# Optimization experiments

Measured on AMD Instinct MI355X. Metric: run time of the kernel, lower is better.

## Reference

```python
import jax, jax.numpy as jnp
import numpy as np
from jax import lax

N_SIN = 3

def _bn(x, g, b, m, v, eps):
    sh = [1] * x.ndim; sh[1] = -1
    r = lambda t: t.reshape(sh)
    return (x - r(m)) / jnp.sqrt(r(v) + eps) * r(g) + r(b)

def _conv2d(x, w, b, padding):
    y = lax.conv_general_dilated(x, w, (1, 1), padding,
                                 dimension_numbers=('NCHW', 'OIHW', 'NCHW'))
    return y + b[None, :, None, None]

def _causal_conv1d(x, w, b):
    k = w.shape[-1]
    y = lax.conv_general_dilated(x, w, (1,), [(k - 1, 0)],
                                 dimension_numbers=('NCH', 'OIH', 'NCH'))
    return y + b[None, :, None]

def _se(x, w1, w2):
    y = x.mean(axis=2)                                   # [B,C] global avg pool
    y = jax.nn.sigmoid(jax.nn.relu(y @ w1.T) @ w2.T)
    return x * y[:, :, None]

def _kan(x, W1, W2, B1, B2):
    # x: [B,din]; per-edge tiny MLP: sin/cos embed -> linear -> silu -> linear
    omega = (2.0 ** jnp.arange(N_SIN)).astype(x.dtype)   # [n_sin]
    ox = x[..., None] * omega                            # [B,din,n_sin]
    feat = jnp.concatenate([x[..., None], jnp.sin(ox), jnp.cos(ox)], axis=-1)  # [B,din,7]
    h = jnp.einsum('bif,ijhf->bijh', feat, W1) + B1[None]  # [B,din,dout,h]
    h = jax.nn.silu(h)
    out = jnp.einsum('bijh,ijh->bij', h, W2[:, :, 0, :]) + B2[None, :, :, 0]
    return out.sum(axis=1)                               # [B,dout]

def _lstm(x, w_ih, w_hh, b_ih, b_hh):
    B, T, E = x.shape
    H = w_hh.shape[1]
    def step(carry, xt):
        h, c = carry
        g = xt @ w_ih.T + h @ w_hh.T + (b_ih + b_hh)
        i, f, gg, o = jnp.split(g, 4, axis=-1)           # torch gate order i,f,g,o
        c = jax.nn.sigmoid(f) * c + jax.nn.sigmoid(i) * jnp.tanh(gg)
        h = jax.nn.sigmoid(o) * jnp.tanh(c)
        return (h, c), h
    init = (jnp.zeros((B, H), x.dtype), jnp.zeros((B, H), x.dtype))
    _, hs = lax.scan(step, init, jnp.swapaxes(x, 0, 1))
    return jnp.swapaxes(hs, 0, 1)                        # [B,T,H]

def _cluster(hidden):
    B, T, H = hidden.shape
    last = hidden[:, -1, :]
    hn = hidden / jnp.maximum(jnp.linalg.norm(hidden, axis=-1, keepdims=True), 1e-8)
    sim = jnp.einsum('bth,bsh->bts', hn, hn)
    sim = jnp.exp(-5.5 * (1.0 - sim))
    sim = sim * (1.0 - jnp.eye(T, dtype=sim.dtype))      # zero diagonal
    # 2-D prefix sums replace the O(T) python loop over block means
    S = jnp.cumsum(jnp.cumsum(sim, axis=1), axis=2)
    Sii = jnp.diagonal(S, axis1=1, axis2=2)[:, :T - 1]   # sum of [:i,:i]
    R = S[:, -1, :T - 1]                                 # sum of [:, :i]
    C = S[:, :T - 1, -1]                                 # sum of [:i, :]
    tot = S[:, -1, -1][:, None]
    i_f = jnp.arange(1, T, dtype=sim.dtype)
    dist = (Sii / i_f**2
            + (tot - R - C + Sii) / (T - i_f)**2
            - (C - Sii) / (i_f * (T - i_f))
            - (R - Sii) / (i_f * (T - i_f)))             # [B,T-1]
    cuts = jnp.argmax(dist, axis=1) + 1                  # [B]
    mask = (jnp.arange(T)[None, :] < cuts[:, None]).astype(hidden.dtype)
    corr = (hidden * mask[:, :, None]).sum(axis=1) / cuts[:, None].astype(hidden.dtype)
    return last, corr

def reference(x, we1, be1, bn_e1_g, bn_e1_b, bn_e1_m, bn_e1_v, we2, be2, bn_e2_g, bn_e2_b, bn_e2_m, bn_e2_v, w_ih, w_hh, b_ih, b_hh, mu_W1, mu_W2, mu_B1, mu_B2, std_W1, std_W2, std_B1, std_B2, muc_W1, muc_W2, muc_B1, muc_B2, stdc_W1, stdc_W2, stdc_B1, stdc_B2, fc_W1, fc_W2, fc_B1, fc_B2, wc1, bc1, bn1_g, bn1_b, bn1_m, bn1_v, se1_w1, se1_w2, wc2, bc2, bn2_g, bn2_b, bn2_m, bn2_v, se2_w1, se2_w2, wc3, bc3, bn3_g, bn3_b, bn3_m, bn3_v, eps1, eps2):
    gelu = lambda t: jax.nn.gelu(t, approximate=False)
    x = jnp.transpose(x, (0, 2, 1))                      # shuffle: [B,T,F]->[B,F,T]
    h2d = _conv2d(x[:, None], we1, be1, 'SAME')          # [B,4E,F,T]
    h2d = gelu(_bn(h2d, bn_e1_g, bn_e1_b, bn_e1_m, bn_e1_v, 1e-5))
    h2d = _conv2d(h2d, we2, be2, 'VALID')                # [B,E,1,T]
    h2d = gelu(_bn(h2d, bn_e2_g, bn_e2_b, bn_e2_m, bn_e2_v, 1e-5))
    x_src = jnp.transpose(h2d[:, :, 0, :], (0, 2, 1))    # [B,T,E]
    hseq = _lstm(x_src, w_ih, w_hh, b_ih, b_hh)          # [B,T,H]
    out, corr = _cluster(hseq)
    mu = _kan(corr, mu_W1, mu_W2, mu_B1, mu_B2)
    std = jax.nn.softplus(_kan(corr, std_W1, std_W2, std_B1, std_B2) - 5.0)
    z = mu + std * eps1
    x_z = jnp.concatenate([out, z], axis=1)              # [B,2H]
    mu_c = _kan(x_z, muc_W1, muc_W2, muc_B1, muc_B2)
    std_c = jax.nn.softplus(_kan(x_z, stdc_W1, stdc_W2, stdc_B1, stdc_B2) - 5.0)
    x1 = mu_c + std_c * eps2                             # dropout = identity (eval)
    x2 = jnp.transpose(x, (0, 2, 1))                     # [B,T,F]: channels = seq_len
    x2 = gelu(_bn(_causal_conv1d(x2, wc1, bc1), bn1_g, bn1_b, bn1_m, bn1_v, 1e-3))
    x2 = _se(x2, se1_w1, se1_w2)
    x2 = gelu(_bn(_causal_conv1d(x2, wc2, bc2), bn2_g, bn2_b, bn2_m, bn2_v, 1e-3))
    x2 = _se(x2, se2_w1, se2_w2)
    x2 = gelu(_bn(_causal_conv1d(x2, wc3, bc3), bn3_g, bn3_b, bn3_m, bn3_v, 1e-3))
    x2 = x2.mean(axis=2)                                 # [B,conv3_nf]
    x_all = jnp.concatenate([x1, x2], axis=1)            # [B, H+conv3_nf]
    return _kan(x_all, fc_W1, fc_W2, fc_B1, fc_B2)       # [B,num_classes]

def setup_inputs():
    key = jax.random.key(0)
    ks = iter(jax.random.split(key, 128))
    f32 = jnp.float32
    def n(shape, s=0.05):
        return s * jax.random.normal(next(ks), shape, f32)
    def bn_params(c):
        g = 1.0 + 0.05 * jax.random.normal(next(ks), (c,), f32)
        b = 0.05 * jax.random.normal(next(ks), (c,), f32)
        m = 0.05 * jax.random.normal(next(ks), (c,), f32)
        v = jax.random.uniform(next(ks), (c,), f32, 0.5, 1.5)
        return g, b, m, v
    def kan_params(din, dout, h=32, feat=1 + 2 * N_SIN):
        s = (2.0 / (feat + h)) ** 0.5
        return (n((din, dout, h, feat), s), n((din, dout, 1, h), s),
                jnp.zeros((din, dout, h), f32), jnp.zeros((din, dout, 1), f32))
    B, T, F_, E, H = 32, 256, 32, 64, 128
    inp = {}
    inp['x'] = jax.random.normal(next(ks), (B, T, F_), f32)
    inp['we1'] = n((4 * E, 1, 1, 8)); inp['be1'] = n((4 * E,))
    inp['bn_e1_g'], inp['bn_e1_b'], inp['bn_e1_m'], inp['bn_e1_v'] = bn_params(4 * E)
    inp['we2'] = n((E, 4 * E, F_, 1)); inp['be2'] = n((E,))
    inp['bn_e2_g'], inp['bn_e2_b'], inp['bn_e2_m'], inp['bn_e2_v'] = bn_params(E)
    inp['w_ih'] = n((4 * H, E)); inp['w_hh'] = n((4 * H, H))
    inp['b_ih'] = n((4 * H,)); inp['b_hh'] = n((4 * H,))
    for nm, (di, do) in [('mu', (H, H)), ('std', (H, H)), ('muc', (2 * H, H)), ('stdc', (2 * H, H)), ('fc', (2 * H, 10))]:
        w1, w2, b1, b2 = kan_params(di, do)
        inp[nm + '_W1'], inp[nm + '_W2'], inp[nm + '_B1'], inp[nm + '_B2'] = w1, w2, b1, b2
    inp['wc1'] = n((128, T, 8)); inp['bc1'] = n((128,))
    inp['bn1_g'], inp['bn1_b'], inp['bn1_m'], inp['bn1_v'] = bn_params(128)
    inp['se1_w1'] = n((8, 128)); inp['se1_w2'] = n((128, 8))
    inp['wc2'] = n((256, 128, 5)); inp['bc2'] = n((256,))
    inp['bn2_g'], inp['bn2_b'], inp['bn2_m'], inp['bn2_v'] = bn_params(256)
    inp['se2_w1'] = n((16, 256)); inp['se2_w2'] = n((256, 16))
    inp['wc3'] = n((128, 256, 3)); inp['bc3'] = n((128,))
    inp['bn3_g'], inp['bn3_b'], inp['bn3_m'], inp['bn3_v'] = bn_params(128)
    inp['eps1'] = jax.random.normal(next(ks), (B, H), f32)
    inp['eps2'] = jax.random.normal(next(ks), (B, H), f32)
    return inp
```

## Files before the change

kernel.cpp:

```cpp
#include <hip/hip_runtime.h>
#include <hip/hip_bf16.h>
#include <math.h>

typedef __hip_bfloat16 bf16;

#define DEV static __device__ __forceinline__

DEV float geluf(float x){ return 0.5f*x*(1.0f + erff(x*0.70710678118654752f)); }
DEV float sigmf(float x){ return 1.0f/(1.0f + __expf(-x)); }
DEV float softplusf(float x){ return (x > 15.f) ? x : log1pf(__expf(x)); }
DEV float tanhfast(float x){ float e = __expf(2.f*x); return fmaf(-2.f, 1.f/(e+1.f), 1.f); }

typedef __attribute__((ext_vector_type(8))) short v8s;
typedef __attribute__((ext_vector_type(4))) float v4f;
typedef _Float16 f16;
typedef f16 h2 __attribute__((ext_vector_type(2)));
typedef f16 f16x8 __attribute__((ext_vector_type(8)));
typedef unsigned u32x4 __attribute__((ext_vector_type(4)));

DEV float dot2f(h2 a, h2 b, float c){
#if __has_builtin(__builtin_amdgcn_fdot2)
  return __builtin_amdgcn_fdot2(a, b, c, false);
#else
  return fmaf((float)a.y, (float)b.y, fmaf((float)a.x, (float)b.x, c));
// ... 150 lines not shown
  for(int i=tid;i<2048;i+=256) w1s[i] = w1f[i];
  b1s[tid] = b1f[tid];
  for(int i=tid;i<39*32;i+=256){
    int r=i>>5, f=i&31; int t=t0-3+r;
    xs[i] = (t>=0 && t<256) ? x[(b*256+t)*32+f] : 0.f;
  }
  __syncthreads();

  int f = tid & 31, tq = tid >> 5;
  int lane = tid & 63, w = tid >> 6;
  int wm = w & 1, wn = w >> 1;
  int m0 = wm*16, n0 = wn*32;
  int l15 = lane & 15, quad = lane >> 4;

  const v8s* Wv = (const v8s*)Wr;

  auto stage = [&](int cc, int buf){
    v8s bw[4];
    #pragma unroll
    for(int i=0;i<4;i++) bw[i] = Wv[cc*1024 + i*256 + tid];
    unsigned short aval[16];
    #pragma unroll
    for(int ol=0;ol<4;ol++){
      int o = cc*4 + ol;
      float wv[8];
      #pragma unroll
      for(int j=0;j<8;j++) wv[j] = w1s[o*8+j];
      float bb = b1s[o];
      #pragma unroll
      for(int i=0;i<4;i++){
        int tl = tq*4 + i;
        float c = bb;
        #pragma unroll
        for(int j=0;j<8;j++) c = fmaf(wv[j], xs[(tl+j)*32+f], c);
        aval[ol*4+i] = ((__hip_bfloat16_raw)__float2bfloat16(geluf(c))).x;
      }
    }
    #pragma unroll
    for(int ol=0;ol<4;ol++){
      #pragma unroll
      for(int i=0;i<4;i++)
        At[buf][(tq*4+i)*136 + ol*32 + f] = aval[ol*4+i];
    }
    #pragma unroll
    for(int i=0;i<4;i++){
      int j = i*256 + tid;
      int ol = j>>8, e = (j&255)>>2, f8 = j&3;
      *(v8s*)&Bt[buf][ol*2560 + e*40 + f8*8] = bw[i];
    }
  };

  stage(0, 0);
  __syncthreads();

  v4f acc0 = {0.f,0.f,0.f,0.f}, acc1 = {0.f,0.f,0.f,0.f};

  for(int c=0;c<64;c++){
    int p = c & 1, q = p ^ 1;
    if(c < 63) stage(c+1, q);
    #pragma unroll
    for(int ol=0;ol<4;ol++){
      v8s av = *(const v8s*)&At[p][(m0+l15)*136 + ol*32 + quad*8];
      v8s b0 = *(const v8s*)&Bt[p][ol*2560 + (n0+l15)*40 + quad*8];
      v8s b1 = *(const v8s*)&Bt[p][ol*2560 + (n0+16+l15)*40 + quad*8];
      acc0 = __builtin_amdgcn_mfma_f32_16x16x32_bf16(av, b0, acc0, 0, 0, 0);
      acc1 = __builtin_amdgcn_mfma_f32_16x16x32_bf16(av, b1, acc1, 0, 0, 0);
    }
    __syncthreads();
  }

  #pragma unroll
  for(int r=0;r<4;r++){
    int t = t0 + m0 + quad*4 + r;
    int e0 = n0 + l15;
    float v0 = geluf(s2e[e0]*acc0[r] + b2e[e0]);
    x_src[((size_t)(b*256+t))*64 + e0] = v0;
    int e1 = e0 + 16;
    float v1 = geluf(s2e[e1]*acc1[r] + b2e[e1]);
    x_src[((size_t)(b*256+t))*64 + e1] = v1;
  }
}

__global__ __launch_bounds__(256) void gates_kernel(
    const float* x_src, const float* wihT, const float* biasg, float* gx)
{
  __shared__ float xsh[32*64];
  int blk = blockIdx.x; int b = blk>>3, t0 = (blk&7)*32;
  int tid = threadIdx.x;
  for(int i=tid;i<2048;i+=256) xsh[i] = x_src[((size_t)b*256+t0)*64 + i];
  __syncthreads();
  int g0 = tid, g1 = tid + 256;
  float acc0[32], acc1[32];
  #pragma unroll
  for(int tt=0;tt<32;tt++){ acc0[tt]=0.f; acc1[tt]=0.f; }
  for(int e=0;e<64;e++){
    float w0 = wihT[e*512+g0], w1 = wihT[e*512+g1];
    #pragma unroll
    for(int tt=0;tt<32;tt++){
      float xv = xsh[tt*64+e];
      acc0[tt] = fmaf(xv, w0, acc0[tt]);
      acc1[tt] = fmaf(xv, w1, acc1[tt]);
    }
  }
  float bg0 = biasg[g0], bg1 = biasg[g1];
  #pragma unroll
  for(int tt=0;tt<32;tt++){
    gx[((size_t)b*256+t0+tt)*512 + g0] = acc0[tt] + bg0;
    gx[((size_t)b*256+t0+tt)*512 + g1] = acc1[tt] + bg1;
  }
}

#define LSTM_STEP(GI, GF, GG, GO, PR, PW, T)                                 \
  {                                                                          \
    const f16x8* hp = (const f16x8*)&hsh[PR][half*64];                       \
    f16x8 hvv[8];                                                            \
    _Pragma("unroll")                                                        \
    for(int q=0;q<8;q++) hvv[q] = hp[q];                                     \
    float si=0.f, sf=0.f, sg=0.f, so=0.f;                                    \
    _Pragma("unroll")                                                        \
    for(int q=0;q<8;q++){                                                    \
      f16x8 Wi = __builtin_bit_cast(f16x8, wi[q]);                           \
      f16x8 Wf = __builtin_bit_cast(f16x8, wf[q]);                           \
      f16x8 Wg = __builtin_bit_cast(f16x8, wg[q]);                           \
      f16x8 Wo = __builtin_bit_cast(f16x8, wo[q]);                           \
      f16x8 hq = hvv[q];                                                     \
      _Pragma("unroll")                                                      \
      for(int j=0;j<4;j++){                                                  \
        h2 hj = geth2(hq, j);                                                \
        si = dot2f(hj, geth2(Wi,j), si);                                     \
        sf = dot2f(hj, geth2(Wf,j), sf);                                     \
        sg = dot2f(hj, geth2(Wg,j), sg);                                     \
        so = dot2f(hj, geth2(Wo,j), so);                                     \
      }                                                                      \
    }                                                                        \
    si += __shfl_xor(si, 32, 64);                                            \
    sf += __shfl_xor(sf, 32, 64);                                            \
    sg += __shfl_xor(sg, 32, 64);                                            \
    so += __shfl_xor(so, 32, 64);                                            \
    float iv = sigmf(si + (GI));                                             \
    float fv = sigmf(sf + (GF));                                             \
    float gv = tanhfast(sg + (GG));                                          \
    float ov = sigmf(so + (GO));                                             \
    c = fmaf(fv, c, iv*gv);                                                  \
    float h = ov*tanhfast(c);                                                \
    if(half == 0){                                                           \
      hsh[PW][n] = (f16)h;                                                   \
      hseq[((size_t)b*256+(T))*128 + n] = h;                                 \
    }                                                                        \
    lds_barrier();                                                           \
  }

__global__ __launch_bounds__(256)
__attribute__((amdgpu_waves_per_eu(1,1)))
void lstm_kernel(
    const float* __restrict__ gates_x, const float* __restrict__ whh16f, float* __restrict__ hseq)
{
  __shared__ __align__(16) f16 hsh[2][128];
  int b = blockIdx.x, tt = threadIdx.x;
  int wave = tt >> 6, lane = tt & 63;
  int half = lane >> 5;
  int n = wave*32 + (lane & 31);

  const u32x4* Wp = (const u32x4*)whh16f;
  u32x4 wi[8], wf[8], wg[8], wo[8];
  #pragma unroll
  for(int q=0;q<8;q++){
    wi[q] = Wp[(size_t)(n      )*16 + half*8 + q];
    wf[q] = Wp[(size_t)(n + 128)*16 + half*8 + q];
    wg[q] = Wp[(size_t)(n + 256)*16 + half*8 + q];
    wo[q] = Wp[(size_t)(n + 384)*16 + half*8 + q];
  }
  asm volatile("" :
    "+v"(wi[0]), "+v"(wi[1]), "+v"(wi[2]), "+v"(wi[3]),
    "+v"(wi[4]), "+v"(wi[5]), "+v"(wi[6]), "+v"(wi[7]),
    "+v"(wf[0]), "+v"(wf[1]), "+v"(wf[2]), "+v"(wf[3]),
    "+v"(wf[4]), "+v"(wf[5]), "+v"(wf[6]), "+v"(wf[7]));
  asm volatile("" :
    "+v"(wg[0]), "+v"(wg[1]), "+v"(wg[2]), "+v"(wg[3]),
    "+v"(wg[4]), "+v"(wg[5]), "+v"(wg[6]), "+v"(wg[7]),
    "+v"(wo[0]), "+v"(wo[1]), "+v"(wo[2]), "+v"(wo[3]),
    "+v"(wo[4]), "+v"(wo[5]), "+v"(wo[6]), "+v"(wo[7]));

  if(tt < 128) hsh[0][tt] = (f16)0.f;
  float c = 0.f;
  const float* gx = gates_x + (size_t)b*256*512;
  float i0v = gx[n], f0v = gx[128+n], g0v = gx[256+n], o0v = gx[384+n];
  float i1v = gx[512+n], f1v = gx[512+128+n], g1v = gx[512+256+n], o1v = gx[512+384+n];
  __syncthreads();
  for(int t=0; t<256; t+=2){
    float i2v=0.f,f2v=0.f,g2v=0.f,o2v=0.f,i3v=0.f,f3v=0.f,g3v=0.f,o3v=0.f;
    if(t+2 < 256){
      const float* gp = gx + (size_t)(t+2)*512;
      i2v = gp[n]; f2v = gp[128+n]; g2v = gp[256+n]; o2v = gp[384+n];
    }
    LSTM_STEP(i0v, f0v, g0v, o0v, 0, 1, t);
    if(t+3 < 256){
      const float* gp = gx + (size_t)(t+3)*512;
      i3v = gp[n]; f3v = gp[128+n]; g3v = gp[256+n]; o3v = gp[384+n];
    }
    LSTM_STEP(i1v, f1v, g1v, o1v, 1, 0, t+1);
    i0v=i2v; f0v=f2v; g0v=g2v; o0v=o2v;
    i1v=i3v; f1v=f3v; g1v=g3v; o1v=o3v;
  }
}

__global__ __launch_bounds__(64) void hn_kernel(const float* hseq, float* hn)
{
  size_t row = blockIdx.x; int lane = threadIdx.x;
  const float* hp = hseq + row*128;
  float v0 = hp[lane], v1 = hp[lane+64];
  float ss = v0*v0 + v1*v1;
  #pragma unroll
  for(int m=1;m<64;m<<=1) ss += __shfl_xor(ss, m, 64);
  float r = 1.f / fmaxf(sqrtf(ss), 1e-8f);
  hn[row*128 + lane]      = v0*r;
  hn[row*128 + 64 + lane] = v1*r;
}

__global__ __launch_bounds__(256) void pc_kernel(const float* hn, float* pcol, float* ccol)
{
  int blk = blockIdx.x; int b = blk>>3, chunk = blk&7;
  int tid = threadIdx.x; int il = tid & 31, ts = tid >> 5;
  int i = chunk*32 + il;
  const float4* hb = (const float4*)(hn + (size_t)b*32768);
  float4 hi[32];
  #pragma unroll
  for(int r=0;r<32;r++) hi[r] = hb[(size_t)i*32 + r];
  float ps=0.f, cs=0.f;
  for(int t=ts*32; t<ts*32+32; t++){
    float dx=0.f, dy=0.f, dz=0.f, dw=0.f;
    #pragma unroll
    for(int r=0;r<32;r++){
      float4 hv = hb[(size_t)t*32 + r];
      dx = fmaf(hi[r].x, hv.x, dx);
      dy = fmaf(hi[r].y, hv.y, dy);
      dz = fmaf(hi[r].z, hv.z, dz);
      dw = fmaf(hi[r].w, hv.w, dw);
    }
    float dot = (dx+dy)+(dz+dw);
    float sim = (t==i) ? 0.f : expf(-5.5f*(1.0f - dot));
    cs += sim;
    if(t < i) ps += sim;
  }
  __shared__ float red[16][32];
  red[ts][il] = ps; red[8+ts][il] = cs;
  __syncthreads();
  if(tid < 32){
    float s=0.f;
    for(int r=0;r<8;r++) s += red[r][tid];
    pcol[b*256 + chunk*32 + tid] = s;
  } else if(tid < 64){
    int c2 = tid - 32; float s=0.f;
    for(int r=0;r<8;r++) s += red[8+r][c2];
    ccol[b*256 + chunk*32 + c2] = s;
  }
}

__global__ __launch_bounds__(256) void cutcorr_kernel(
    const float* pcol, const float* ccol, const float* hseq,
    float* last, float* corr, int* cuts)
{
  int b = blockIdx.x, tid = threadIdx.x;
  __shared__ float D[256], RC[256], dist[256];
  __shared__ int cutsh;
  if(tid == 0){
    float d=0.f, r=0.f;
    for(int i=0;i<256;i++){
      d += 2.f*pcol[b*256+i]; D[i]=d;
      r += ccol[b*256+i];     RC[i]=r;
    }
  }
  __syncthreads();
  float tot = RC[255];
  if(tid < 255){
    float Dv = D[tid], Rv = RC[tid];
    float i_f = (float)(tid+1), j_f = 256.f - i_f;
    dist[tid] = Dv/(i_f*i_f) + (tot - 2.f*Rv + Dv)/(j_f*j_f) - 2.f*(Rv - Dv)/(i_f*j_f);
  }
  __syncthreads();
  if(tid == 0){
    float best = dist[0]; int bi = 0;
    for(int i=1;i<255;i++) if(dist[i] > best){ best = dist[i]; bi = i; }
    cutsh = bi + 1; cuts[b] = cutsh;
  }
  __syncthreads();
  int cut = cutsh;
  int k = tid & 127, half = tid >> 7;
  float s = 0.f;
  for(int t=half; t<cut; t+=2) s += hseq[((size_t)b*256+t)*128 + k];
  __shared__ float partial[2][128];
  partial[half][k] = s;
  __syncthreads();
  if(tid < 128){
    corr[b*128+tid] = (partial[0][tid] + partial[1][tid]) / (float)cut;
    last[b*128+tid] = hseq[((size_t)b*256+255)*128 + tid];
  }
}

__global__ __launch_bounds__(256) void feat_kernel(const float* xin, float* feat, int n)
{
  int idx = blockIdx.x*256 + threadIdx.x;
  if(idx >= n) return;
  float xv = xin[idx];
  float* fp = feat + (size_t)idx*7;
  fp[0]=xv;
  fp[1]=sinf(xv); fp[2]=sinf(2.f*xv); fp[3]=sinf(4.f*xv);
  fp[4]=cosf(xv); fp[5]=cosf(2.f*xv); fp[6]=cosf(4.f*xv);
}

__global__ __launch_bounds__(256) void kanp_kernel(
    const float* __restrict__ feat, const float* __restrict__ W1,
    const float* __restrict__ B1, const float* __restrict__ W2,
    int din, int dout, float* __restrict__ partial)
{
  __shared__ float feat_s[32*225];
  __shared__ float red[8][32];
  int j = blockIdx.x, ic = blockIdx.y;
  int i0 = ic*32;
  int tid = threadIdx.x;
  int b = tid & 31, hg = tid >> 5;
  for(int q=tid; q<1792; q+=256){
    int br = q/56, qq = q - br*56;
    float4 v = *(const float4*)(feat + ((size_t)br*din + i0)*7 + qq*4);
    float* d = &feat_s[br*225 + qq*4];
    d[0]=v.x; d[1]=v.y; d[2]=v.z; d[3]=v.w;
  }
  __syncthreads();
  float acc = 0.f;
  const float* fb = &feat_s[b*225];
  for(int ii=0; ii<32; ii++){
    int i = i0 + ii;
    size_t hbase = ((size_t)i*dout + j)*32 + hg*4;
    const float4* w1p = (const float4*)(W1 + ((size_t)i*dout + j)*224 + hg*28);
    float w1a[28];
    #pragma unroll
    for(int q=0;q<7;q++) *(float4*)&w1a[q*4] = w1p[q];
    float4 b1v = *(const float4*)(B1 + hbase);
    float4 w2v = *(const float4*)(W2 + hbase);
    float f[7];
    #pragma unroll
    for(int q=0;q<7;q++) f[q] = fb[ii*7+q];
    float b1a[4] = {b1v.x, b1v.y, b1v.z, b1v.w};
    float w2a[4] = {w2v.x, w2v.y, w2v.z, w2v.w};
    #pragma unroll
    for(int hh=0;hh<4;hh++){
      float hv = b1a[hh];
      #pragma unroll
      for(int q=0;q<7;q++) hv = fmaf(f[q], w1a[hh*7+q], hv);
      float sv = hv / (1.f + __expf(-hv));
      acc = fmaf(sv, w2a[hh], acc);
    }
  }
  red[hg][b] = acc;
  __syncthreads();
  if(tid < 32){
    float s = 0.f;
    #pragma unroll
    for(int q=0;q<8;q++) s += red[q][tid];
    partial[((size_t)ic*32 + tid)*dout + j] = s;
  }
}

__global__ __launch_bounds__(256) void kanr_kernel(
    const float* __restrict__ partial, const float* __restrict__ b2s,
    int NI, int dout, float* __restrict__ outp)
{
  int idx = blockIdx.x*256 + threadIdx.x;
  if(idx >= 32*dout) return;
  int b = idx / dout, j = idx - b*dout;
  float s = b2s[j];
  for(int ic=0; ic<NI; ic++) s += partial[((size_t)ic*32 + b)*dout + j];
  outp[idx] = s;
}

__global__ __launch_bounds__(256) void zmix_kernel(
    const float* muo, const float* stdo, const float* eps1, const float* last, float* xz)
{
  int idx = blockIdx.x*256 + threadIdx.x;
  if(idx >= 4096) return;
  int b = idx >> 7, k = idx & 127;
  float z = muo[idx] + softplusf(stdo[idx] - 5.f)*eps1[idx];
  xz[b*256 + k]       = last[idx];
  xz[b*256 + 128 + k] = z;
}

__global__ __launch_bounds__(256) void xall_kernel(
    const float* muco, const float* stdco, const float* eps2, const float* x2f, float* xa)
{
  int idx = blockIdx.x*256 + threadIdx.x;
  if(idx >= 4096) return;
  int b = idx >> 7, k = idx & 127;
  xa[b*256 + k]       = muco[idx] + softplusf(stdco[idx] - 5.f)*eps2[idx];
  xa[b*256 + 128 + k] = x2f[idx];
}

template<int CIN, int K, int COUT, int NCH, int LG>
__global__ __launch_bounds__(COUT*LG, 1) void convp_kernel(
    const float* __restrict__ xin, const float* __restrict__ w, float* __restrict__ part)
{
  constexpr int L = 32/LG;
  constexpr int CCH = CIN/NCH;
  __shared__ float xsh[CCH*32];
  int b = blockIdx.x, ch = blockIdx.y;
  int tid = threadIdx.x;
  for(int i=tid; i<CCH*32; i+=COUT*LG) xsh[i] = xin[((size_t)b*CIN + ch*CCH)*32 + i];
  __syncthreads();
  int o = tid / LG, lh = tid % LG;
  int l0 = lh*L;
  float acc[L];
  #pragma unroll
  for(int j=0;j<L;j++) acc[j]=0.f;
  const float* wrow = w + ((size_t)o*CIN + ch*CCH)*K;
  for(int c=0;c<CCH;c++){
    float wv[K];
    #pragma unroll
    for(int k=0;k<K;k++) wv[k] = wrow[c*K + k];
    float xr[L+K-1];
    #pragma unroll
    for(int i=0;i<L+K-1;i++){
      int li = l0 - (K-1) + i;
      xr[i] = (li>=0) ? xsh[c*32+li] : 0.f;
    }
    #pragma unroll
    for(int j=0;j<L;j++){
      #pragma unroll
      for(int k=0;k<K;k++) acc[j] = fmaf(xr[j+k], wv[k], acc[j]);
    }
  }
  float* pp = part + (((size_t)ch*32 + b)*COUT + o)*32 + l0;
  #pragma unroll
  for(int j=0;j<L;j++) pp[j] = acc[j];
}

template<int C, int R, int NP>
__global__ __launch_bounds__(C,1) void sef_kernel(
    const float* __restrict__ part, const float* __restrict__ epi_s, const float* __restrict__ epi_b,
    const float* __restrict__ w1, const float* __restrict__ w2, float* __restrict__ out)
{
  __shared__ float mean[C];
  __shared__ float y1[R];
  int b = blockIdx.x, c = threadIdx.x;
  float g[32];
  #pragma unroll
  for(int l=0;l<32;l++) g[l]=0.f;
  for(int p=0;p<NP;p++){
    const float* pp = part + (((size_t)p*32 + b)*C + c)*32;
    #pragma unroll
    for(int l=0;l<32;l++) g[l] += pp[l];
  }
  float s = epi_s[c], bb = epi_b[c];
  float m = 0.f;
  #pragma unroll
  for(int l=0;l<32;l++){ g[l] = geluf(s*g[l]+bb); m += g[l]; }
  mean[c] = m*(1.f/32.f);
  __syncthreads();
  if(c < R){
    float t=0.f;
    for(int k=0;k<C;k++) t = fmaf(mean[k], w1[c*C+k], t);
    y1[c] = fmaxf(t,0.f);
  }
  __syncthreads();
  float t=0.f;
  #pragma unroll
  for(int k=0;k<R;k++) t = fmaf(y1[k], w2[c*R+k], t);
  float sc = sigmf(t);
  float* op = out + ((size_t)b*C + c)*32;
  #pragma unroll
  for(int l=0;l<32;l++) op[l] = g[l]*sc;
}

__global__ __launch_bounds__(128,1) void mean3f_kernel(
    const float* __restrict__ part, const float* __restrict__ epi_s, const float* __restrict__ epi_b,
    float* __restrict__ x2f)
{
  int b = blockIdx.x, c = threadIdx.x;
  float g[32];
  #pragma unroll
  for(int l=0;l<32;l++) g[l]=0.f;
  for(int p=0;p<8;p++){
    const float* pp = part + (((size_t)p*32 + b)*128 + c)*32;
    #pragma unroll
    for(int l=0;l<32;l++) g[l] += pp[l];
  }
  float s = epi_s[c], bb = epi_b[c];
  float m = 0.f;
  #pragma unroll
  for(int l=0;l<32;l++) m += geluf(s*g[l]+bb);
  x2f[b*128 + c] = m*(1.f/32.f);
}

extern "C" void kernel_launch(void* const* d_in, const int* in_sizes, int n_in,
                              void* d_out, int out_size, void* d_ws, size_t ws_size,
                              hipStream_t stream)
{
  const float* x    = (const float*)d_in[0];
  const float* we1  = (const float*)d_in[1];
  const float* be1  = (const float*)d_in[2];
  const float* e1g  = (const float*)d_in[3];
  const float* e1b  = (const float*)d_in[4];
  const float* e1m  = (const float*)d_in[5];
  const float* e1v  = (const float*)d_in[6];
  const float* we2  = (const float*)d_in[7];
  const float* be2  = (const float*)d_in[8];
  const float* e2g  = (const float*)d_in[9];
  const float* e2b  = (const float*)d_in[10];
  const float* e2m  = (const float*)d_in[11];
  const float* e2v  = (const float*)d_in[12];
  const float* wih  = (const float*)d_in[13];
  const float* whh  = (const float*)d_in[14];
  const float* bih  = (const float*)d_in[15];
  const float* bhh  = (const float*)d_in[16];
  const float* muW1 = (const float*)d_in[17];
  const float* muW2 = (const float*)d_in[18];
  const float* muB1 = (const float*)d_in[19];
  const float* muB2 = (const float*)d_in[20];
  const float* sdW1 = (const float*)d_in[21];
  const float* sdW2 = (const float*)d_in[22];
  const float* sdB1 = (const float*)d_in[23];
  const float* sdB2 = (const float*)d_in[24];
  const float* mcW1 = (const float*)d_in[25];
  const float* mcW2 = (const float*)d_in[26];
  const float* mcB1 = (const float*)d_in[27];
  const float* mcB2 = (const float*)d_in[28];
  const float* scW1 = (const float*)d_in[29];
  const float* scW2 = (const float*)d_in[30];
  const float* scB1 = (const float*)d_in[31];
  const float* scB2 = (const float*)d_in[32];
  const float* fcW1 = (const float*)d_in[33];
  const float* fcW2 = (const float*)d_in[34];
  const float* fcB1 = (const float*)d_in[35];
  const float* fcB2 = (const float*)d_in[36];
  const float* wc1  = (const float*)d_in[37];
  const float* bc1  = (const float*)d_in[38];
  const float* c1g  = (const float*)d_in[39];
  const float* c1b  = (const float*)d_in[40];
  const float* c1m  = (const float*)d_in[41];
  const float* c1v  = (const float*)d_in[42];
  const float* se1w1= (const float*)d_in[43];
  const float* se1w2= (const float*)d_in[44];
  const float* wc2  = (const float*)d_in[45];
  const float* bc2  = (const float*)d_in[46];
  const float* c2g  = (const float*)d_in[47];
  const float* c2b  = (const float*)d_in[48];
  const float* c2m  = (const float*)d_in[49];
  const float* c2v  = (const float*)d_in[50];
  const float* se2w1= (const float*)d_in[51];
  const float* se2w2= (const float*)d_in[52];
  const float* wc3  = (const float*)d_in[53];
  const float* bc3  = (const float*)d_in[54];
  const float* c3g  = (const float*)d_in[55];
  const float* c3b  = (const float*)d_in[56];
  const float* c3m  = (const float*)d_in[57];
  const float* c3v  = (const float*)d_in[58];
  const float* eps1 = (const float*)d_in[59];
  const float* eps2 = (const float*)d_in[60];

  float* ws = (float*)d_ws;
  float* part = ws + OFF_GX;
  float* kp   = ws + OFF_KP;
  float* b2s  = ws + OFF_B2S;

  prep_kernel<<<2448, 256, 0, stream>>>(we1, be1, e1g,e1b,e1m,e1v,
      we2, be2,e2g,e2b,e2m,e2v, wih,whh,bih,bhh,
      bc1,c1g,c1b,c1m,c1v, bc2,c2g,c2b,c2m,c2v, bc3,c3g,c3b,c3m,c3v,
      muB2, sdB2, mcB2, scB2, fcB2, ws);

  encoder_kernel<<<256, 256, 0, stream>>>(x, ws+OFF_W1F, ws+OFF_B1F,
      ws+OFF_S2E, ws+OFF_B2E, (const bf16*)(ws+OFF_WE2B), ws+OFF_XSRC);

  gates_kernel<<<256, 256, 0, stream>>>(ws+OFF_XSRC, ws+OFF_WIHT, ws+OFF_BIASG, ws+OFF_GX);
  lstm_kernel<<<32, 256, 0, stream>>>(ws+OFF_GX, ws+OFF_WHHT, ws+OFF_HSEQ);

  hn_kernel<<<8192, 64, 0, stream>>>(ws+OFF_HSEQ, ws+OFF_HN);
  pc_kernel<<<256, 256, 0, stream>>>(ws+OFF_HN, ws+OFF_PCOL, ws+OFF_CCOL);
  cutcorr_kernel<<<32, 256, 0, stream>>>(ws+OFF_PCOL, ws+OFF_CCOL, ws+OFF_HSEQ,
      ws+OFF_LAST, ws+OFF_CORR, (int*)(ws+OFF_CUTS));

  feat_kernel<<<16, 256, 0, stream>>>(ws+OFF_CORR, ws+OFF_FEATA, 4096);
  kanp_kernel<<<dim3(128,4), 256, 0, stream>>>(ws+OFF_FEATA, muW1, muB1, muW2, 128, 128, kp);
  kanr_kernel<<<16, 256, 0, stream>>>(kp, b2s+0, 4, 128, ws+OFF_MUO);
  kanp_kernel<<<dim3(128,4), 256, 0, stream>>>(ws+OFF_FEATA, sdW1, sdB1, sdW2, 128, 128, kp);
  kanr_kernel<<<16, 256, 0, stream>>>(kp, b2s+128, 4, 128, ws+OFF_STDO);
  zmix_kernel<<<16, 256, 0, stream>>>(ws+OFF_MUO, ws+OFF_STDO, eps1, ws+OFF_LAST, ws+OFF_XZ);
  feat_kernel<<<32, 256, 0, stream>>>(ws+OFF_XZ, ws+OFF_FEATB, 8192);
  kanp_kernel<<<dim3(128,8), 256, 0, stream>>>(ws+OFF_FEATB, mcW1, mcB1, mcW2, 256, 128, kp);
  kanr_kernel<<<16, 256, 0, stream>>>(kp, b2s+256, 8, 128, ws+OFF_MUCO);
  kanp_kernel<<<dim3(128,8), 256, 0, stream>>>(ws+OFF_FEATB, scW1, scB1, scW2, 256, 128, kp);
  kanr_kernel<<<16, 256, 0, stream>>>(kp, b2s+384, 8, 128, ws+OFF_STDCO);

  convp_kernel<256,8,128,8,2><<<dim3(32,8), 256, 0, stream>>>(x, wc1, part);
  sef_kernel<128,8,8><<<32, 128, 0, stream>>>(part, ws+OFF_EPI1S, ws+OFF_EPI1B, se1w1, se1w2, ws+OFF_XC1);
  convp_kernel<128,5,256,4,1><<<dim3(32,4), 256, 0, stream>>>(ws+OFF_XC1, wc2, part);
  sef_kernel<256,16,4><<<32, 256, 0, stream>>>(part, ws+OFF_EPI2S, ws+OFF_EPI2B, se2w1, se2w2, ws+OFF_XC2);
  convp_kernel<256,3,128,8,2><<<dim3(32,8), 256, 0, stream>>>(ws+OFF_XC2, wc3, part);
  mean3f_kernel<<<32, 128, 0, stream>>>(part, ws+OFF_EPI3S, ws+OFF_EPI3B, ws+OFF_X2F);

  xall_kernel<<<16, 256, 0, stream>>>(ws+OFF_MUCO, ws+OFF_STDCO, eps2, ws+OFF_X2F, ws+OFF_XALL);
  feat_kernel<<<32, 256, 0, stream>>>(ws+OFF_XALL, ws+OFF_FEATC, 8192);
  kanp_kernel<<<dim3(10,8), 256, 0, stream>>>(ws+OFF_FEATC, fcW1, fcB1, fcW2, 256, 10, kp);
  kanr_kernel<<<2, 256, 0, stream>>>(kp, b2s+512, 8, 10, (float*)d_out);
}
```

Measured before the change: 966.7 us.

## Run conv branch alongside LSTM in one kernel; pair mu/std KAN launches

Fuses the three-stage conv/SE branch into extra blocks of the LSTM kernel, so the conv work runs on idle CUs while the 32 sequential LSTM blocks execute. Each conv block now does a whole batch item's conv chain in LDS instead of a split-K partial/reduce scheme across six launches. The mu/std KAN pairs are also merged into single launches using a z grid dimension, with their reductions fused into the zmix/xall combine steps. The cost is about 50KB of LDS per block on the LSTM path and much less parallelism per conv block. If the conv blocks run longer than the LSTM, they become the critical path.

Result: faster. 875.1 us (-9.5%).

```diff
diff --git a/kernel.cpp b/kernel.cpp
--- a/kernel.cpp
+++ b/kernel.cpp
@@ -326,55 +326,192 @@
 
 __global__ __launch_bounds__(256)
 __attribute__((amdgpu_waves_per_eu(1,1)))
-void lstm_kernel(
-    const float* __restrict__ gates_x, const float* __restrict__ whh16f, float* __restrict__ hseq)
+void lstm_conv_kernel(
+    const float* __restrict__ gates_x, const float* __restrict__ whh16f, float* __restrict__ hseq,
+    const float* __restrict__ x,
+    const float* __restrict__ wc1, const float* __restrict__ wc2, const float* __restrict__ wc3,
+    const float* __restrict__ epi1s, const float* __restrict__ epi1b,
+    const float* __restrict__ epi2s, const float* __restrict__ epi2b,
+    const float* __restrict__ epi3s, const float* __restrict__ epi3b,
+    const float* __restrict__ se1w1, const float* __restrict__ se1w2,
+    const float* __restrict__ se2w1, const float* __restrict__ se2w2,
+    float* __restrict__ x2f)
 {
   __shared__ __align__(16) f16 hsh[2][128];
-  int b = blockIdx.x, tt = threadIdx.x;
-  int wave = tt >> 6, lane = tt & 63;
-  int half = lane >> 5;
-  int n = wave*32 + (lane & 31);
-
-  const u32x4* Wp = (const u32x4*)whh16f;
-  u32x4 wi[8], wf[8], wg[8], wo[8];
-  #pragma unroll
-  for(int q=0;q<8;q++){
-    wi[q] = Wp[(size_t)(n      )*16 + half*8 + q];
-    wf[q] = Wp[(size_t)(n + 128)*16 + half*8 + q];
-    wg[q] = Wp[(size_t)(n + 256)*16 + half*8 + q];
-    wo[q] = Wp[(size_t)(n + 384)*16 + half*8 + q];
-  }
-  asm volatile("" :
-    "+v"(wi[0]), "+v"(wi[1]), "+v"(wi[2]), "+v"(wi[3]),
-    "+v"(wi[4]), "+v"(wi[5]), "+v"(wi[6]), "+v"(wi[7]),
-    "+v"(wf[0]), "+v"(wf[1]), "+v"(wf[2]), "+v"(wf[3]),
-    "+v"(wf[4]), "+v"(wf[5]), "+v"(wf[6]), "+v"(wf[7]));
-  asm volatile("" :
-    "+v"(wg[0]), "+v"(wg[1]), "+v"(wg[2]), "+v"(wg[3]),
-    "+v"(wg[4]), "+v"(wg[5]), "+v"(wg[6]), "+v"(wg[7]),
-    "+v"(wo[0]), "+v"(wo[1]), "+v"(wo[2]), "+v"(wo[3]),
-    "+v"(wo[4]), "+v"(wo[5]), "+v"(wo[6]), "+v"(wo[7]));
-
-  if(tt < 128) hsh[0][tt] = (f16)0.f;
-  float c = 0.f;
-  const float* gx = gates_x + (size_t)b*256*512;
-  float i0v = gx[n], f0v = gx[128+n], g0v = gx[256+n], o0v = gx[384+n];
-  float i1v = gx[512+n], f1v = gx[512+128+n], g1v = gx[512+256+n], o1v = gx[512+384+n];
-  __syncthreads();
-  for(int t=0; t<256; t+=2){
-    float i2v=0.f,f2v=0.f,g2v=0.f,o2v=0.f,i3v=0.f,f3v=0.f,g3v=0.f,o3v=0.f;
-    if(t+2 < 256){
-      const float* gp = gx + (size_t)(t+2)*512;
-      i2v = gp[n]; f2v = gp[128+n]; g2v = gp[256+n]; o2v = gp[384+n];
-    }
-    LSTM_STEP(i0v, f0v, g0v, o0v, 0, 1, t);
-    if(t+3 < 256){
-      const float* gp = gx + (size_t)(t+3)*512;
-      i3v = gp[n]; f3v = gp[128+n]; g3v = gp[256+n]; o3v = gp[384+n];
-    }
-    LSTM_STEP(i1v, f1v, g1v, o1v, 1, 0, t+1);
-    i0v=i2v; f0v=f2v; g0v=g2v; o0v=o2v;
-    i1v=i3v; f1v=f3v; g1v=g3v; o1v=o3v;
+  __shared__ float bufA[8192];
+  __shared__ float bufB[4096];
+  __shared__ float msh[256];
+  __shared__ float ysh[16];
+
+  int tid = threadIdx.x;
+  if(blockIdx.x < 32){
+    int b = blockIdx.x;
+    int wave = tid >> 6, lane = tid & 63;
+    int half = lane >> 5;
+    int n = wave*32 + (lane & 31);
+
+    const u32x4* Wp = (const u32x4*)whh16f;
+    u32x4 wi[8], wf[8], wg[8], wo[8];
+    #pragma unroll
+    for(int q=0;q<8;q++){
+      wi[q] = Wp[(size_t)(n      )*16 + half*8 + q];
+      wf[q] = Wp[(size_t)(n + 128)*16 + half*8 + q];
+      wg[q] = Wp[(size_t)(n + 256)*16 + half*8 + q];
+      wo[q] = Wp[(size_t)(n + 384)*16 + half*8 + q];
+    }
+    asm volatile("" :
+      "+v"(wi[0]), "+v"(wi[1]), "+v"(wi[2]), "+v"(wi[3]),
+      "+v"(wi[4]), "+v"(wi[5]), "+v"(wi[6]), "+v"(wi[7]),
+      "+v"(wf[0]), "+v"(wf[1]), "+v"(wf[2]), "+v"(wf[3]),
+      "+v"(wf[4]), "+v"(wf[5]), "+v"(wf[6]), "+v"(wf[7]));
+    asm volatile("" :
+      "+v"(wg[0]), "+v"(wg[1]), "+v"(wg[2]), "+v"(wg[3]),
+      "+v"(wg[4]), "+v"(wg[5]), "+v"(wg[6]), "+v"(wg[7]),
+      "+v"(wo[0]), "+v"(wo[1]), "+v"(wo[2]), "+v"(wo[3]),
+      "+v"(wo[4]), "+v"(wo[5]), "+v"(wo[6]), "+v"(wo[7]));
+
+    if(tid < 128) hsh[0][tid] = (f16)0.f;
+    float c = 0.f;
+    const float* gx = gates_x + (size_t)b*256*512;
+    float i0v = gx[n], f0v = gx[128+n], g0v = gx[256+n], o0v = gx[384+n];
+    float i1v = gx[512+n], f1v = gx[512+128+n], g1v = gx[512+256+n], o1v = gx[512+384+n];
+    __syncthreads();
+    for(int t=0; t<256; t+=2){
+      float i2v=0.f,f2v=0.f,g2v=0.f,o2v=0.f,i3v=0.f,f3v=0.f,g3v=0.f,o3v=0.f;
+      if(t+2 < 256){
+        const float* gp = gx + (size_t)(t+2)*512;
+        i2v = gp[n]; f2v = gp[128+n]; g2v = gp[256+n]; o2v = gp[384+n];
+      }
+      LSTM_STEP(i0v, f0v, g0v, o0v, 0, 1, t);
+      if(t+3 < 256){
+        const float* gp = gx + (size_t)(t+3)*512;
+        i3v = gp[n]; f3v = gp[128+n]; g3v = gp[256+n]; o3v = gp[384+n];
+      }
+      LSTM_STEP(i1v, f1v, g1v, o1v, 1, 0, t+1);
+      i0v=i2v; f0v=f2v; g0v=g2v; o0v=o2v;
+      i1v=i3v; f1v=f3v; g1v=g3v; o1v=o3v;
+    }
+  } else {
+    int cb = blockIdx.x - 32;
+    for(int i=tid; i<8192; i+=256) bufA[i] = x[(size_t)cb*8192 + i];
+    __syncthreads();
+
+    {
+      int o = tid >> 1, lh = tid & 1, l0 = lh*16;
+      float acc[16];
+      #pragma unroll
+      for(int j=0;j<16;j++) acc[j]=0.f;
+      const float* wrow = wc1 + (size_t)o*2048;
+      for(int c=0;c<256;c++){
+        float wv[8];
+        #pragma unroll
+        for(int k=0;k<8;k++) wv[k] = wrow[c*8+k];
+        float xr[23];
+        #pragma unroll
+        for(int i=0;i<23;i++){
+          int li = l0 - 7 + i;
+          xr[i] = (li>=0) ? bufA[c*32+li] : 0.f;
+        }
+        #pragma unroll
+        for(int j=0;j<16;j++){
+          #pragma unroll
+          for(int k=0;k<8;k++) acc[j] = fmaf(xr[j+k], wv[k], acc[j]);
+        }
+      }
+      float s = epi1s[o], bb = epi1b[o];
+      float g[16]; float m = 0.f;
+      #pragma unroll
+      for(int j=0;j<16;j++){ g[j] = geluf(s*acc[j]+bb); m += g[j]; }
+      m += __shfl_xor(m, 1, 64);
+      if(lh==0) msh[o] = m*(1.f/32.f);
+      __syncthreads();
+      if(tid < 8){
+        float t2=0.f;
+        for(int k=0;k<128;k++) t2 = fmaf(msh[k], se1w1[tid*128+k], t2);
+        ysh[tid] = fmaxf(t2, 0.f);
+      }
+      __syncthreads();
+      float t2=0.f;
+      #pragma unroll
+      for(int k=0;k<8;k++) t2 = fmaf(ysh[k], se1w2[o*8+k], t2);
+      float sc = sigmf(t2);
+      #pragma unroll
+      for(int j=0;j<16;j++) bufB[o*32 + l0 + j] = g[j]*sc;
+      __syncthreads();
+    }
+
+    {
+      int o = tid;
+      float acc[32];
+      #pragma unroll
+      for(int j=0;j<32;j++) acc[j]=0.f;
+      const float* wrow = wc2 + (size_t)o*640;
+      for(int c=0;c<128;c++){
+        float wv[5];
+        #pragma unroll
+        for(int k=0;k<5;k++) wv[k] = wrow[c*5+k];
+        float xr[36];
+        #pragma unroll
+        for(int i=0;i<36;i++){
+          int li = i - 4;
+          xr[i] = (li>=0) ? bufB[c*32+li] : 0.f;
+        }
+        #pragma unroll
+        for(int j=0;j<32;j++){
+          #pragma unroll
+          for(int k=0;k<5;k++) acc[j] = fmaf(xr[j+k], wv[k], acc[j]);
+        }
+      }
+      float s = epi2s[o], bb = epi2b[o];
+      float m = 0.f;
+      #pragma unroll
+      for(int j=0;j<32;j++){ acc[j] = geluf(s*acc[j]+bb); m += acc[j]; }
+      msh[o] = m*(1.f/32.f);
+      __syncthreads();
+      if(tid < 16){
+        float t2=0.f;
+        for(int k=0;k<256;k++) t2 = fmaf(msh[k], se2w1[tid*256+k], t2);
+        ysh[tid] = fmaxf(t2, 0.f);
+      }
+      __syncthreads();
+      float t2=0.f;
+      #pragma unroll
+      for(int k=0;k<16;k++) t2 = fmaf(ysh[k], se2w2[o*16+k], t2);
+      float sc = sigmf(t2);
+      #pragma unroll
+      for(int j=0;j<32;j++) bufA[o*32 + j] = acc[j]*sc;
+      __syncthreads();
+    }
+
+    {
+      int o = tid >> 1, lh = tid & 1, l0 = lh*16;
+      float acc[16];
+      #pragma unroll
+      for(int j=0;j<16;j++) acc[j]=0.f;
+      const float* wrow = wc3 + (size_t)o*768;
+      for(int c=0;c<256;c++){
+        float wv[3];
+        #pragma unroll
+        for(int k=0;k<3;k++) wv[k] = wrow[c*3+k];
+        float xr[18];
+        #pragma unroll
+        for(int i=0;i<18;i++){
+          int li = l0 - 2 + i;
+          xr[i] = (li>=0) ? bufA[c*32+li] : 0.f;
+        }
+        #pragma unroll
+        for(int j=0;j<16;j++){
+          #pragma unroll
+          for(int k=0;k<3;k++) acc[j] = fmaf(xr[j+k], wv[k], acc[j]);
+        }
+      }
+      float s = epi3s[o], bb = epi3b[o];
+      float m = 0.f;
+      #pragma unroll
+      for(int j=0;j<16;j++) m += geluf(s*acc[j]+bb);
+      m += __shfl_xor(m, 1, 64);
+      if(lh==0) x2f[cb*128 + o] = m*(1.f/32.f);
+    }
   }
 }
 
@@ -480,6 +617,65 @@
   fp[0]=xv;
   fp[1]=sinf(xv); fp[2]=sinf(2.f*xv); fp[3]=sinf(4.f*xv);
   fp[4]=cosf(xv); fp[5]=cosf(2.f*xv); fp[6]=cosf(4.f*xv);
+}
+
+__global__ __launch_bounds__(256) void kanp2_kernel(
+    const float* __restrict__ feat,
+    const float* __restrict__ W1a, const float* __restrict__ B1a, const float* __restrict__ W2a,
+    const float* __restrict__ W1b, const float* __restrict__ B1b, const float* __restrict__ W2b,
+    int din, int dout, float* __restrict__ partial, int pstride)
+{
+  __shared__ float feat_s[32*225];
+  __shared__ float red[8][32];
+  int z = blockIdx.z;
+  const float* W1 = z ? W1b : W1a;
+  const float* B1 = z ? B1b : B1a;
+  const float* W2 = z ? W2b : W2a;
+  partial += (size_t)z * pstride;
+  int j = blockIdx.x, ic = blockIdx.y;
+  int i0 = ic*32;
+  int tid = threadIdx.x;
+  int b = tid & 31, hg = tid >> 5;
+  for(int q=tid; q<1792; q+=256){
+    int br = q/56, qq = q - br*56;
+    float4 v = *(const float4*)(feat + ((size_t)br*din + i0)*7 + qq*4);
+    float* d = &feat_s[br*225 + qq*4];
+    d[0]=v.x; d[1]=v.y; d[2]=v.z; d[3]=v.w;
+  }
+  __syncthreads();
+  float acc = 0.f;
+  const float* fb = &feat_s[b*225];
+  for(int ii=0; ii<32; ii++){
+    int i = i0 + ii;
+    size_t hbase = ((size_t)i*dout + j)*32 + hg*4;
+    const float4* w1p = (const float4*)(W1 + ((size_t)i*dout + j)*224 + hg*28);
+    float w1a[28];
+    #pragma unroll
+    for(int q=0;q<7;q++) *(float4*)&w1a[q*4] = w1p[q];
+    float4 b1v = *(const float4*)(B1 + hbase);
+    float4 w2v = *(const float4*)(W2 + hbase);
+    float f[7];
+    #pragma unroll
+    for(int q=0;q<7;q++) f[q] = fb[ii*7+q];
+    float b1a[4] = {b1v.x, b1v.y, b1v.z, b1v.w};
+    float w2a[4] = {w2v.x, w2v.y, w2v.z, w2v.w};
+    #pragma unroll
+    for(int hh=0;hh<4;hh++){
+      float hv = b1a[hh];
+      #pragma unroll
+      for(int q=0;q<7;q++) hv = fmaf(f[q], w1a[hh*7+q], hv);
+      float sv = hv / (1.f + __expf(-hv));
+      acc = fmaf(sv, w2a[hh], acc);
+    }
+  }
+  red[hg][b] = acc;
+  __syncthreads();
+  if(tid < 32){
+    float s = 0.f;
+    #pragma unroll
+    for(int q=0;q<8;q++) s += red[q][tid];
+    partial[((size_t)ic*32 + tid)*dout + j] = s;
+  }
 }
 
 __global__ __launch_bounds__(256) void kanp_kernel(
@@ -547,120 +743,39 @@
   outp[idx] = s;
 }
 
-__global__ __launch_bounds__(256) void zmix_kernel(
-    const float* muo, const float* stdo, const float* eps1, const float* last, float* xz)
+__global__ __launch_bounds__(256) void kanrz_kernel(
+    const float* __restrict__ kp, const float* __restrict__ b2s,
+    const float* __restrict__ eps1, const float* __restrict__ last, float* __restrict__ xz)
 {
   int idx = blockIdx.x*256 + threadIdx.x;
   if(idx >= 4096) return;
-  int b = idx >> 7, k = idx & 127;
-  float z = muo[idx] + softplusf(stdo[idx] - 5.f)*eps1[idx];
-  xz[b*256 + k]       = last[idx];
-  xz[b*256 + 128 + k] = z;
-}
-
-__global__ __launch_bounds__(256) void xall_kernel(
-    const float* muco, const float* stdco, const float* eps2, const float* x2f, float* xa)
+  int b = idx >> 7, j = idx & 127;
+  float mu = b2s[j], sd = b2s[128+j];
+  #pragma unroll
+  for(int ic=0; ic<4; ic++){
+    mu += kp[((size_t)ic*32 + b)*128 + j];
+    sd += kp[16384 + ((size_t)ic*32 + b)*128 + j];
+  }
+  float z = mu + softplusf(sd - 5.f)*eps1[idx];
+  xz[b*256 + j]       = last[idx];
+  xz[b*256 + 128 + j] = z;
+}
+
+__global__ __launch_bounds__(256) void kanrx_kernel(
+    const float* __restrict__ kp, const float* __restrict__ b2s,
+    const float* __restrict__ eps2, const float* __restrict__ x2f, float* __restrict__ xa)
 {
   int idx = blockIdx.x*256 + threadIdx.x;
   if(idx >= 4096) return;
-  int b = idx >> 7, k = idx & 127;
-  xa[b*256 + k]       = muco[idx] + softplusf(stdco[idx] - 5.f)*eps2[idx];
-  xa[b*256 + 128 + k] = x2f[idx];
-}
-
-template<int CIN, int K, int COUT, int NCH, int LG>
-__global__ __launch_bounds__(COUT*LG, 1) void convp_kernel(
-    const float* __restrict__ xin, const float* __restrict__ w, float* __restrict__ part)
-{
-  constexpr int L = 32/LG;
-  constexpr int CCH = CIN/NCH;
-  __shared__ float xsh[CCH*32];
-  int b = blockIdx.x, ch = blockIdx.y;
-  int tid = threadIdx.x;
-  for(int i=tid; i<CCH*32; i+=COUT*LG) xsh[i] = xin[((size_t)b*CIN + ch*CCH)*32 + i];
-  __syncthreads();
-  int o = tid / LG, lh = tid % LG;
-  int l0 = lh*L;
-  float acc[L];
+  int b = idx >> 7, j = idx & 127;
+  float mu = b2s[256+j], sd = b2s[384+j];
   #pragma unroll
-  for(int j=0;j<L;j++) acc[j]=0.f;
-  const float* wrow = w + ((size_t)o*CIN + ch*CCH)*K;
-  for(int c=0;c<CCH;c++){
-    float wv[K];
-    #pragma unroll
-    for(int k=0;k<K;k++) wv[k] = wrow[c*K + k];
-    float xr[L+K-1];
-    #pragma unroll
-    for(int i=0;i<L+K-1;i++){
-      int li = l0 - (K-1) + i;
-      xr[i] = (li>=0) ? xsh[c*32+li] : 0.f;
-    }
-    #pragma unroll
-    for(int j=0;j<L;j++){
-      #pragma unroll
-      for(int k=0;k<K;k++) acc[j] = fmaf(xr[j+k], wv[k], acc[j]);
-    }
-  }
-  float* pp = part + (((size_t)ch*32 + b)*COUT + o)*32 + l0;
-  #pragma unroll
-  for(int j=0;j<L;j++) pp[j] = acc[j];
-}
-
-template<int C, int R, int NP>
-__global__ __launch_bounds__(C,1) void sef_kernel(
-    const float* __restrict__ part, const float* __restrict__ epi_s, const float* __restrict__ epi_b,
-    const float* __restrict__ w1, const float* __restrict__ w2, float* __restrict__ out)
-{
-  __shared__ float mean[C];
-  __shared__ float y1[R];
-  int b = blockIdx.x, c = threadIdx.x;
-  float g[32];
-  #pragma unroll
-  for(int l=0;l<32;l++) g[l]=0.f;
-  for(int p=0;p<NP;p++){
-    const float* pp = part + (((size_t)p*32 + b)*C + c)*32;
-    #pragma unroll
-    for(int l=0;l<32;l++) g[l] += pp[l];
-  }
-  float s = epi_s[c], bb = epi_b[c];
-  float m = 0.f;
-  #pragma unroll
-  for(int l=0;l<32;l++){ g[l] = geluf(s*g[l]+bb); m += g[l]; }
-  mean[c] = m*(1.f/32.f);
-  __syncthreads();
-  if(c < R){
-    float t=0.f;
-    for(int k=0;k<C;k++) t = fmaf(mean[k], w1[c*C+k], t);
-    y1[c] = fmaxf(t,0.f);
-  }
-  __syncthreads();
-  float t=0.f;
-  #pragma unroll
-  for(int k=0;k<R;k++) t = fmaf(y1[k], w2[c*R+k], t);
-  float sc = sigmf(t);
-  float* op = out + ((size_t)b*C + c)*32;
-  #pragma unroll
-  for(int l=0;l<32;l++) op[l] = g[l]*sc;
-}
-
-__global__ __launch_bounds__(128,1) void mean3f_kernel(
-    const float* __restrict__ part, const float* __restrict__ epi_s, const float* __restrict__ epi_b,
-    float* __restrict__ x2f)
-{
-  int b = blockIdx.x, c = threadIdx.x;
-  float g[32];
-  #pragma unroll
-  for(int l=0;l<32;l++) g[l]=0.f;
-  for(int p=0;p<8;p++){
-    const float* pp = part + (((size_t)p*32 + b)*128 + c)*32;
-    #pragma unroll
-    for(int l=0;l<32;l++) g[l] += pp[l];
-  }
-  float s = epi_s[c], bb = epi_b[c];
-  float m = 0.f;
-  #pragma unroll
-  for(int l=0;l<32;l++) m += geluf(s*g[l]+bb);
-  x2f[b*128 + c] = m*(1.f/32.f);
+  for(int ic=0; ic<8; ic++){
+    mu += kp[((size_t)ic*32 + b)*128 + j];
+    sd += kp[32768 + ((size_t)ic*32 + b)*128 + j];
+  }
+  xa[b*256 + j]       = mu + softplusf(sd - 5.f)*eps2[idx];
+  xa[b*256 + 128 + j] = x2f[idx];
 }
 
 extern "C" void kernel_launch(void* const* d_in, const int* in_sizes, int n_in,
@@ -730,8 +845,8 @@
   const float* eps2 = (const float*)d_in[60];
 
   float* ws = (float*)d_ws;
-  float* part = ws + OFF_GX;
   float* kp   = ws + OFF_KP;
+  float* kp2  = ws + OFF_GX;
   float* b2s  = ws + OFF_B2S;
 
   prep_kernel<<<2448, 256, 0, stream>>>(we1, be1, e1g,e1b,e1m,e1v,
@@ -743,7 +858,11 @@
       ws+OFF_S2E, ws+OFF_B2E, (const bf16*)(ws+OFF_WE2B), ws+OFF_XSRC);
 
   gates_kernel<<<256, 256, 0, stream>>>(ws+OFF_XSRC, ws+OFF_WIHT, ws+OFF_BIASG, ws+OFF_GX);
-  lstm_kernel<<<32, 256, 0, stream>>>(ws+OFF_GX, ws+OFF_WHHT, ws+OFF_HSEQ);
+
+  lstm_conv_kernel<<<64, 256, 0, stream>>>(ws+OFF_GX, ws+OFF_WHHT, ws+OFF_HSEQ,
+      x, wc1, wc2, wc3,
+      ws+OFF_EPI1S, ws+OFF_EPI1B, ws+OFF_EPI2S, ws+OFF_EPI2B, ws+OFF_EPI3S, ws+OFF_EPI3B,
+      se1w1, se1w2, se2w1, se2w2, ws+OFF_X2F);
 
   hn_kernel<<<8192, 64, 0, stream>>>(ws+OFF_HSEQ, ws+OFF_HN);
   pc_kernel<<<256, 256, 0, stream>>>(ws+OFF_HN, ws+OFF_PCOL, ws+OFF_CCOL);
@@ -751,25 +870,15 @@
       ws+OFF_LAST, ws+OFF_CORR, (int*)(ws+OFF_CUTS));
 
   feat_kernel<<<16, 256, 0, stream>>>(ws+OFF_CORR, ws+OFF_FEATA, 4096);
-  kanp_kernel<<<dim3(128,4), 256, 0, stream>>>(ws+OFF_FEATA, muW1, muB1, muW2, 128, 128, kp);
-  kanr_kernel<<<16, 256, 0, stream>>>(kp, b2s+0, 4, 128, ws+OFF_MUO);
-  kanp_kernel<<<dim3(128,4), 256, 0, stream>>>(ws+OFF_FEATA, sdW1, sdB1, sdW2, 128, 128, kp);
-  kanr_kernel<<<16, 256, 0, stream>>>(kp, b2s+128, 4, 128, ws+OFF_STDO);
-  zmix_kernel<<<16, 256, 0, stream>>>(ws+OFF_MUO, ws+OFF_STDO, eps1, ws+OFF_LAST, ws+OFF_XZ);
+  kanp2_kernel<<<dim3(128,4,2), 256, 0, stream>>>(ws+OFF_FEATA,
+      muW1, muB1, muW2, sdW1, sdB1, sdW2, 128, 128, kp, 16384);
+  kanrz_kernel<<<16, 256, 0, stream>>>(kp, b2s, eps1, ws+OFF_LAST, ws+OFF_XZ);
+
   feat_kernel<<<32, 256, 0, stream>>>(ws+OFF_XZ, ws+OFF_FEATB, 8192);
-  kanp_kernel<<<dim3(128,8), 256, 0, stream>>>(ws+OFF_FEATB, mcW1, mcB1, mcW2, 256, 128, kp);
-  kanr_kernel<<<16, 256, 0, stream>>>(kp, b2s+256, 8, 128, ws+OFF_MUCO);
-  kanp_kernel<<<dim3(128,8), 256, 0, stream>>>(ws+OFF_FEATB, scW1, scB1, scW2, 256, 128, kp);
-  kanr_kernel<<<16, 256, 0, stream>>>(kp, b2s+384, 8, 128, ws+OFF_STDCO);
-
-  convp_kernel<256,8,128,8,2><<<dim3(32,8), 256, 0, stream>>>(x, wc1, part);
-  sef_kernel<128,8,8><<<32, 128, 0, stream>>>(part, ws+OFF_EPI1S, ws+OFF_EPI1B, se1w1, se1w2, ws+OFF_XC1);
-  convp_kernel<128,5,256,4,1><<<dim3(32,4), 256, 0, stream>>>(ws+OFF_XC1, wc2, part);
-  sef_kernel<256,16,4><<<32, 256, 0, stream>>>(part, ws+OFF_EPI2S, ws+OFF_EPI2B, se2w1, se2w2, ws+OFF_XC2);
-  convp_kernel<256,3,128,8,2><<<dim3(32,8), 256, 0, stream>>>(ws+OFF_XC2, wc3, part);
-  mean3f_kernel<<<32, 128, 0, stream>>>(part, ws+OFF_EPI3S, ws+OFF_EPI3B, ws+OFF_X2F);
-
-  xall_kernel<<<16, 256, 0, stream>>>(ws+OFF_MUCO, ws+OFF_STDCO, eps2, ws+OFF_X2F, ws+OFF_XALL);
+  kanp2_kernel<<<dim3(128,8,2), 256, 0, stream>>>(ws+OFF_FEATB,
+      mcW1, mcB1, mcW2, scW1, scB1, scW2, 256, 128, kp2, 32768);
+  kanrx_kernel<<<16, 256, 0, stream>>>(kp2, b2s, eps2, ws+OFF_X2F, ws+OFF_XALL);
+
   feat_kernel<<<32, 256, 0, stream>>>(ws+OFF_XALL, ws+OFF_FEATC, 8192);
   kanp_kernel<<<dim3(10,8), 256, 0, stream>>>(ws+OFF_FEATC, fcW1, fcB1, fcW2, 256, 10, kp);
   kanr_kernel<<<2, 256, 0, stream>>>(kp, b2s+512, 8, 10, (float*)d_out);
```
